# Kernel optimization log

Measured on AMD Instinct MI355X. Metric: run time of the kernel, lower is better.

Reference implementation:

```python
import jax, jax.numpy as jnp
import numpy as np

EPS = 1e-07  # DIoULoss eps


def setup_inputs() -> dict:
    key = jax.random.key(0)
    k1, k2, k3, k4, k5 = jax.random.split(key, 5)
    B, Q = 32, 131072
    # valid xyxy boxes: uniform centers in [0,100), sizes in [1,51)
    def make_boxes(kc, ks):
        c = jax.random.uniform(kc, (B, Q, 2), dtype=jnp.float32) * 100.0
        wh = jax.random.uniform(ks, (B, Q, 2), dtype=jnp.float32) * 50.0 + 1.0
        return jnp.concatenate([c - wh / 2, c + wh / 2], axis=-1)
    inputs = make_boxes(k1, k2)
    targets = make_boxes(k3, k4)
    mask = jax.random.randint(k5, (B, Q), 0, 2).astype(jnp.bool_)
    num_boxes = 2097152
    return {"inputs": inputs, "targets": targets, "mask": mask, "num_boxes": num_boxes}


def _diou_loss(b1, b2):
    # b1, b2: (N, 4) xyxy. Per-pair GIoU == diagonal of the original NxN matrix.
    a1 = (b1[:, 2] - b1[:, 0]) * (b1[:, 3] - b1[:, 1])
    a2 = (b2[:, 2] - b2[:, 0]) * (b2[:, 3] - b2[:, 1])
    lt = jnp.maximum(b1[:, :2], b2[:, :2])
    rb = jnp.minimum(b1[:, 2:], b2[:, 2:])
    wh = jnp.clip(rb - lt, 0.0)
    inter = wh[:, 0] * wh[:, 1]
    union = a1 + a2 - inter
    iou = inter / union
    lt_c = jnp.minimum(b1[:, :2], b2[:, :2])
    rb_c = jnp.maximum(b1[:, 2:], b2[:, 2:])
    wh_c = rb_c - lt_c  # boxes are valid so enclose extent >= 0
    area_c = wh_c[:, 0] * wh_c[:, 1]
    giou = iou - (area_c - union) / area_c
    # DIoU penalty: squared center distance / squared enclosing diagonal
    c1 = (b1[:, :2] + b1[:, 2:]) * 0.5
    c2 = (b2[:, :2] + b2[:, 2:]) * 0.5
    d2 = jnp.sum((c1 - c2) ** 2, axis=1)
    diag2 = wh_c[:, 0] ** 2 + wh_c[:, 1] ** 2
    diou = giou - d2 / (diag2 + EPS)
    return 1.0 - diou


def reference(inputs, targets, mask, num_boxes):
    B, Q, _ = inputs.shape
    loss = _diou_loss(inputs.reshape(-1, 4), targets.reshape(-1, 4)).reshape(B, Q)
    loss = loss * mask.astype(loss.dtype)
    # reduction='mean' with num_boxes provided -> sum / num_boxes
    return loss.sum() / num_boxes
```

## Files before the change

kernel.cpp:

```cpp
#include <hip/hip_runtime.h>

#define DIOU_EPS 1e-7f

constexpr int BLOCK = 256;
constexpr int GRID  = 1024;
constexpr int VPT   = 4;
constexpr int TILE  = BLOCK * VPT;

__device__ __forceinline__ float rcp_fast(float x) {
    return __builtin_amdgcn_rcpf(x);
}

__device__ __forceinline__ float diou_elem(float4 a, float4 b, int m) {
    float a1 = (a.z - a.x) * (a.w - a.y);
    float a2 = (b.z - b.x) * (b.w - b.y);

    float iw = fmaxf(fminf(a.z, b.z) - fmaxf(a.x, b.x), 0.0f);
    float ih = fmaxf(fminf(a.w, b.w) - fmaxf(a.y, b.y), 0.0f);
    float inter = iw * ih;
    float uni = a1 + a2 - inter;

    float wc = fmaxf(a.z, b.z) - fminf(a.x, b.x);
    float hc = fmaxf(a.w, b.w) - fminf(a.y, b.y);
    float area_c = wc * hc;

    float dx = (a.x + a.z - b.x - b.z) * 0.5f;
    float dy = (a.y + a.w - b.y - b.w) * 0.5f;
    float d2 = dx * dx + dy * dy;
    float diag2 = wc * wc + hc * hc;

    float loss = 2.0f - inter * rcp_fast(uni)
                      - uni   * rcp_fast(area_c)
                      + d2    * rcp_fast(diag2 + DIOU_EPS);

    return (m != 0) ? loss : 0.0f;
}

struct Tile {
    float4 A[VPT];
    float4 B[VPT];
    int4   M;
};

__device__ __forceinline__ void load_tile(const float4* __restrict__ boxes1,
                                          const float4* __restrict__ boxes2,
                                          const int4* __restrict__ mask4,
                                          long long e0, Tile& T) {
    #pragma unroll
    for (int j = 0; j < VPT; ++j) T.A[j] = boxes1[e0 + j];
    #pragma unroll
    for (int j = 0; j < VPT; ++j) T.B[j] = boxes2[e0 + j];
    T.M = mask4[e0 >> 2];
}

__global__ __launch_bounds__(BLOCK, 4) void diou_partial_kernel(
    const float4* __restrict__ boxes1,
    const float4* __restrict__ boxes2,
    const int* __restrict__ mask,
    float* __restrict__ ws,
    int n)
{
    const int t = threadIdx.x;
    const int4* mask4 = (const int4*)mask;
    const long long nfull = n / TILE;

    float acc = 0.0f;

    Tile cur, nxt;
    long long tb = blockIdx.x;
    bool any = tb < nfull;
    if (any) load_tile(boxes1, boxes2, mask4, tb * TILE + (long long)t * VPT, cur);

    while (any) {
        long long tn = tb + GRID;
        bool hn = tn < nfull;
        if (hn) load_tile(boxes1, boxes2, mask4, tn * TILE + (long long)t * VPT, nxt);

        int mm[VPT] = {cur.M.x, cur.M.y, cur.M.z, cur.M.w};
        #pragma unroll
        for (int j = 0; j < VPT; ++j) acc += diou_elem(cur.A[j], cur.B[j], mm[j]);

        cur = nxt;
        tb = tn;
        any = hn;
    }

    for (long long i = nfull * TILE + (long long)blockIdx.x * BLOCK + t; i < n;
         i += (long long)GRID * BLOCK)
        acc += diou_elem(boxes1[i], boxes2[i], mask[i]);

    #pragma unroll
    for (int off = 32; off > 0; off >>= 1)
        acc += __shfl_down(acc, off, 64);

    __shared__ float wsum[BLOCK / 64];
    if ((t & 63) == 0) wsum[t >> 6] = acc;
    __syncthreads();
    if (t == 0) ws[blockIdx.x] = wsum[0] + wsum[1] + wsum[2] + wsum[3];
}

__global__ __launch_bounds__(BLOCK) void finalize_kernel(
    const float* __restrict__ ws,
    const int* __restrict__ num_boxes,
    float* __restrict__ out)
{
    const int t = threadIdx.x;
    float a = 0.0f;
    #pragma unroll
    for (int i = 0; i < GRID / BLOCK; ++i) a += ws[i * BLOCK + t];

    #pragma unroll
    for (int off = 32; off > 0; off >>= 1)
        a += __shfl_down(a, off, 64);

    __shared__ float wsum[BLOCK / 64];
    if ((t & 63) == 0) wsum[t >> 6] = a;
    __syncthreads();
    if (t == 0)
        out[0] = (wsum[0] + wsum[1] + wsum[2] + wsum[3]) / (float)num_boxes[0];
}

extern "C" void kernel_launch(void* const* d_in, const int* in_sizes, int n_in,
                              void* d_out, int out_size, void* d_ws, size_t ws_size,
                              hipStream_t stream) {
    const float4* boxes1 = (const float4*)d_in[0];
    const float4* boxes2 = (const float4*)d_in[1];
    const int* mask = (const int*)d_in[2];
    const int* num_boxes = (const int*)d_in[3];

    float* out = (float*)d_out;
    float* partials = (float*)d_ws;
    int n = in_sizes[2];

    diou_partial_kernel<<<GRID, BLOCK, 0, stream>>>(boxes1, boxes2, mask, partials, n);
    finalize_kernel<<<1, BLOCK, 0, stream>>>(partials, num_boxes, out);
}
```

Baseline: 163.2 us.

## Replace persistent grid-stride loop with one-tile-per-block launch

After: 164.6 us, median of 2. About the same (+0.8%).

```diff
diff --git a/kernel.cpp b/kernel.cpp
--- a/kernel.cpp
+++ b/kernel.cpp
@@ -3,7 +3,6 @@
 #define DIOU_EPS 1e-7f
 
 constexpr int BLOCK = 256;
-constexpr int GRID  = 1024;
 constexpr int VPT   = 4;
 constexpr int TILE  = BLOCK * VPT;
 
@@ -36,24 +35,7 @@
     return (m != 0) ? loss : 0.0f;
 }
 
-struct Tile {
-    float4 A[VPT];
-    float4 B[VPT];
-    int4   M;
-};
-
-__device__ __forceinline__ void load_tile(const float4* __restrict__ boxes1,
-                                          const float4* __restrict__ boxes2,
-                                          const int4* __restrict__ mask4,
-                                          long long e0, Tile& T) {
-    #pragma unroll
-    for (int j = 0; j < VPT; ++j) T.A[j] = boxes1[e0 + j];
-    #pragma unroll
-    for (int j = 0; j < VPT; ++j) T.B[j] = boxes2[e0 + j];
-    T.M = mask4[e0 >> 2];
-}
-
-__global__ __launch_bounds__(BLOCK, 4) void diou_partial_kernel(
+__global__ __launch_bounds__(BLOCK, 8) void diou_partial_kernel(
     const float4* __restrict__ boxes1,
     const float4* __restrict__ boxes2,
     const int* __restrict__ mask,
@@ -61,33 +43,29 @@
     int n)
 {
     const int t = threadIdx.x;
-    const int4* mask4 = (const int4*)mask;
-    const long long nfull = n / TILE;
-
+    const long long base = (long long)blockIdx.x * TILE;
     float acc = 0.0f;
 
-    Tile cur, nxt;
-    long long tb = blockIdx.x;
-    bool any = tb < nfull;
-    if (any) load_tile(boxes1, boxes2, mask4, tb * TILE + (long long)t * VPT, cur);
+    if (base + TILE <= n) {
+        const long long e0 = base + (long long)t * VPT;
+        float4 A[VPT], B[VPT];
+        #pragma unroll
+        for (int j = 0; j < VPT; ++j) A[j] = boxes1[e0 + j];
+        #pragma unroll
+        for (int j = 0; j < VPT; ++j) B[j] = boxes2[e0 + j];
+        int4 M4 = ((const int4*)mask)[e0 >> 2];
 
-    while (any) {
-        long long tn = tb + GRID;
-        bool hn = tn < nfull;
-        if (hn) load_tile(boxes1, boxes2, mask4, tn * TILE + (long long)t * VPT, nxt);
+        __builtin_amdgcn_sched_barrier(0);
 
-        int mm[VPT] = {cur.M.x, cur.M.y, cur.M.z, cur.M.w};
+        int mm[VPT] = {M4.x, M4.y, M4.z, M4.w};
         #pragma unroll
-        for (int j = 0; j < VPT; ++j) acc += diou_elem(cur.A[j], cur.B[j], mm[j]);
-
-        cur = nxt;
-        tb = tn;
-        any = hn;
+        for (int j = 0; j < VPT; ++j) acc += diou_elem(A[j], B[j], mm[j]);
+    } else {
+        for (int j = 0; j < VPT; ++j) {
+            long long i = base + (long long)t * VPT + j;
+            if (i < n) acc += diou_elem(boxes1[i], boxes2[i], mask[i]);
+        }
     }
-
-    for (long long i = nfull * TILE + (long long)blockIdx.x * BLOCK + t; i < n;
-         i += (long long)GRID * BLOCK)
-        acc += diou_elem(boxes1[i], boxes2[i], mask[i]);
 
     #pragma unroll
     for (int off = 32; off > 0; off >>= 1)
@@ -102,12 +80,12 @@
 __global__ __launch_bounds__(BLOCK) void finalize_kernel(
     const float* __restrict__ ws,
     const int* __restrict__ num_boxes,
-    float* __restrict__ out)
+    float* __restrict__ out,
+    int nblocks)
 {
     const int t = threadIdx.x;
     float a = 0.0f;
-    #pragma unroll
-    for (int i = 0; i < GRID / BLOCK; ++i) a += ws[i * BLOCK + t];
+    for (int i = t; i < nblocks; i += BLOCK) a += ws[i];
 
     #pragma unroll
     for (int off = 32; off > 0; off >>= 1)
@@ -132,6 +110,7 @@
     float* partials = (float*)d_ws;
     int n = in_sizes[2];
 
-    diou_partial_kernel<<<GRID, BLOCK, 0, stream>>>(boxes1, boxes2, mask, partials, n);
-    finalize_kernel<<<1, BLOCK, 0, stream>>>(partials, num_boxes, out);
+    int grid = (n + TILE - 1) / TILE;
+    diou_partial_kernel<<<grid, BLOCK, 0, stream>>>(boxes1, boxes2, mask, partials, n);
+    finalize_kernel<<<1, BLOCK, 0, stream>>>(partials, num_boxes, out, grid);
 }
```
